# Kernel tuning notes

Measured on AMD Instinct MI355X. Metric: run time of the kernel, lower is better.

Reference implementation:

```python
import jax, jax.numpy as jnp
import numpy as np

N, E, P = 50000, 500000, 10000
F_IN, H, C = 128, 256, 1


def gat_conv(x, src, dst, W, a_s, a_d, b):
    # single-head GATConv (PyG): h = x W; e_ij = LeakyReLU(a_s.h_j + a_d.h_i)
    n = x.shape[0]
    h = x @ W                              # [n, out]
    es = h @ a_s                           # [n]
    ed = h @ a_d                           # [n]
    logits = jax.nn.leaky_relu(es[src] + ed[dst], 0.2)   # [E']
    m = jax.ops.segment_max(logits, dst, num_segments=n)
    p = jnp.exp(logits - m[dst])
    denom = jax.ops.segment_sum(p, dst, num_segments=n)
    alpha = p / denom[dst]                 # edge-softmax over incoming edges
    out = jax.ops.segment_sum(h[src] * alpha[:, None], dst, num_segments=n)
    return out + b


def setup_inputs():
    key = jax.random.key(0)
    ks = jax.random.split(key, 14)
    inp = {
        "features": jax.random.normal(ks[0], (N, F_IN), jnp.float32),
        "edge_index": jax.random.randint(ks[1], (2, E), 0, N, dtype=jnp.int32),
        "mask": jax.random.randint(ks[2], (P, 2), 0, N, dtype=jnp.int32),
        "W1": jax.random.normal(ks[3], (F_IN, H), jnp.float32) / np.sqrt(F_IN),
        "a_src1": jax.random.normal(ks[4], (H,), jnp.float32) / np.sqrt(H),
        "a_dst1": jax.random.normal(ks[5], (H,), jnp.float32) / np.sqrt(H),
        "b1": jnp.zeros((H,), jnp.float32),
        "W2": jax.random.normal(ks[6], (H, F_IN), jnp.float32) / np.sqrt(H),
        "a_src2": jax.random.normal(ks[7], (F_IN,), jnp.float32) / np.sqrt(F_IN),
        "a_dst2": jax.random.normal(ks[8], (F_IN,), jnp.float32) / np.sqrt(F_IN),
        "b2": jnp.zeros((F_IN,), jnp.float32),
        "Wl": jax.random.normal(ks[9], (2 * F_IN, C), jnp.float32) / np.sqrt(2 * F_IN),
        "bl": jnp.zeros((C,), jnp.float32),
    }
    return inp


def reference(features, edge_index, mask, W1, a_src1, a_dst1, b1, W2, a_src2, a_dst2, b2, Wl, bl):
    n = features.shape[0]
    loop = jnp.arange(n, dtype=edge_index.dtype)   # PyG add_self_loops=True
    src = jnp.concatenate([edge_index[0], loop])
    dst = jnp.concatenate([edge_index[1], loop])
    h = gat_conv(features, src, dst, W1, a_src1, a_dst1, b1)   # [N, H]
    h = jax.nn.relu(h)                                         # dropout=0.0
    h = gat_conv(h, src, dst, W2, a_src2, a_dst2, b2)          # [N, F_IN]
    mT = mask.T
    p1 = jax.lax.stop_gradient(h[mT[0]])   # .detach() in original
    p2 = jax.lax.stop_gradient(h[mT[1]])
    z = jnp.concatenate([p1, p2], axis=1)  # [P, 2*F_IN]
    return jax.nn.sigmoid(z @ Wl + bl)
```

## Files before the change

### kernel.cpp

```cpp
#include <hip/hip_runtime.h>
#include <hip/hip_bf16.h>
#include <math.h>

#define NN 50000
#define NE 500000
#define NP 10000
#define FIN 128
#define HD 256
#define NE_TOT (NE + NN)

typedef __attribute__((ext_vector_type(8))) short bf16x8;
typedef __attribute__((ext_vector_type(4))) float f32x4;
typedef __attribute__((ext_vector_type(2))) float f32x2;

__device__ inline unsigned short f2bf(float f) {
  unsigned int u = __float_as_uint(f);
  unsigned int r = (u + 0x7fffu + ((u >> 16) & 1u)) >> 16;
  return (unsigned short)r;
}

__device__ inline float bflo(unsigned int u) { return __uint_as_float(u << 16); }
__device__ inline float bfhi(unsigned int u) { return __uint_as_float(u & 0xffff0000u); }

__device__ inline unsigned char f2fp8(float v) {
  int pk = __builtin_amdgcn_cvt_pk_fp8_f32(v, v, 0, false);
  return (unsigned char)(pk & 0xff);
}

__global__ void init_prep(int* __restrict__ deg,
                          const float* __restrict__ W1, const float* __restrict__ W2,
                          unsigned short* __restrict__ W1T, unsigned short* __restrict__ W2T) {
  int idx = blockIdx.x * 256 + threadIdx.x;
  if (idx < NN) deg[idx] = 1;
  if (idx < FIN * HD) {
    int n = idx / FIN, k = idx - n * FIN;
    W1T[idx] = f2bf(W1[(size_t)k * HD + n]);
    int n2 = idx / HD, k2 = idx - n2 * HD;
    W2T[idx] = f2bf(W2[(size_t)k2 * FIN + n2]);
  }
}

__global__ void hist_kernel(const int* __restrict__ dst, int* __restrict__ deg) {
  int e = blockIdx.x * blockDim.x + threadIdx.x;
  if (e < NE) atomicAdd(&deg[dst[e]], 1);
}

__global__ void scan_phase1(const int* __restrict__ deg, int* __restrict__ incl,
                            int* __restrict__ bsum, int n) {
  __shared__ int tmp[256];
  int i = blockIdx.x * 256 + threadIdx.x;
  int v = (i < n) ? deg[i] : 0;
  tmp[threadIdx.x] = v;
  __syncthreads();
  for (int off = 1; off < 256; off <<= 1) {
    int t = (threadIdx.x >= off) ? tmp[threadIdx.x - off] : 0;
    __syncthreads();
    tmp[threadIdx.x] += t;
    __syncthreads();
  }
  if (i < n) incl[i] = tmp[threadIdx.x];
  if (threadIdx.x == 255) bsum[blockIdx.x] = tmp[255];
}

__global__ void scan_phase3(const int* __restrict__ deg, const int* __restrict__ incl,
                            const int* __restrict__ bsum, int* __restrict__ row_ptr,
                            int* __restrict__ cursor, int n, int total, int nb) {
  __shared__ int wsum[4];
  int bid = blockIdx.x;
  int v = (threadIdx.x < bid && threadIdx.x < nb) ? bsum[threadIdx.x] : 0;
#pragma unroll
  for (int off = 32; off; off >>= 1) v += __shfl_xor(v, off, 64);
  if ((threadIdx.x & 63) == 0) wsum[threadIdx.x >> 6] = v;
  __syncthreads();
  int prefix = wsum[0] + wsum[1] + wsum[2] + wsum[3];

  int i = bid * 256 + threadIdx.x;
  if (i < n) {
    int excl = incl[i] - deg[i] + prefix;
    row_ptr[i] = excl;
    cursor[i] = excl;
  }
  if (i == n) row_ptr[n] = total;
}

__global__ void scatter_kernel(const int* __restrict__ src, const int* __restrict__ dst,
                               int* __restrict__ cursor, int* __restrict__ ssrc) {
  int e = blockIdx.x * blockDim.x + threadIdx.x;
  if (e < NE) {
    int pos = atomicAdd(&cursor[dst[e]], 1);
    ssrc[pos] = src[e];
  } else if (e < NE_TOT) {
    int i = e - NE;
    int pos = atomicAdd(&cursor[i], 1);
    ssrc[pos] = i;
  }
}

template <int BN, int KTOT, bool A_BF16, bool C_FP8>
__global__ __launch_bounds__(512)
void mfma_gemm(const void* __restrict__ Aptr, const unsigned short* __restrict__ BT,
               void* __restrict__ Cptr, const float* __restrict__ a_s,
               const float* __restrict__ a_d, float* __restrict__ es, float* __restrict__ ed,
               int M) {
  constexpr int LDK = 72;
  constexpr int CN = BN / 2;
  constexpr int NT = CN / 16;
  __shared__ unsigned short As[128][LDK];
  __shared__ unsigned short Bs[BN][LDK];
  __shared__ float esl[128][2];
  __shared__ float edl[128][2];
  const int tid = threadIdx.x;
  const int wave = tid >> 6;
  const int lane = tid & 63;
  const int quad = lane >> 4;
  const int l16 = lane & 15;
  const int wrow = wave >> 1;
  const int wcol = wave & 1;
  const int row0 = blockIdx.x * 128;

  f32x4 acc[2][NT] = {};

  for (int k0 = 0; k0 < KTOT; k0 += 64) {
#pragma unroll
    for (int p = 0; p < 4; p++) {
      int m = p * 32 + (tid >> 4);
      int k4 = (tid & 15) * 4;
      int gr = row0 + m;
      uint2 pk = make_uint2(0u, 0u);
      if (gr < M) {
        if (A_BF16) {
          pk = *(const uint2*)((const unsigned short*)Aptr + (size_t)gr * KTOT + k0 + k4);
        } else {
          float4 v = *(const float4*)((const float*)Aptr + (size_t)gr * KTOT + k0 + k4);
          pk.x = (unsigned int)f2bf(v.x) | ((unsigned int)f2bf(v.y) << 16);
          pk.y = (unsigned int)f2bf(v.z) | ((unsigned int)f2bf(v.w) << 16);
        }
      }
      *(uint2*)&As[m][k4] = pk;
    }
#pragma unroll
    for (int p = 0; p < BN / 64; p++) {
      int n = p * 64 + (tid >> 3);
      int k8 = (tid & 7) * 8;
      *(uint4*)&Bs[n][k8] = *(const uint4*)(BT + (size_t)n * KTOT + k0 + k8);
    }
    __syncthreads();
#pragma unroll
    for (int ks = 0; ks < 2; ks++) {
      bf16x8 afrag[2];
#pragma unroll
      for (int rt = 0; rt < 2; rt++)
        afrag[rt] = *(const bf16x8*)&As[wrow * 32 + rt * 16 + l16][ks * 32 + quad * 8];
#pragma unroll
      for (int ct = 0; ct < NT; ct++) {
        bf16x8 bfrag = *(const bf16x8*)&Bs[wcol * CN + ct * 16 + l16][ks * 32 + quad * 8];
#pragma unroll
        for (int rt = 0; rt < 2; rt++)
          acc[rt][ct] = __builtin_amdgcn_mfma_f32_16x16x32_bf16(afrag[rt], bfrag, acc[rt][ct], 0, 0, 0);
      }
    }
    __syncthreads();
  }

  float asv[NT], adv[NT];
#pragma unroll
  for (int ct = 0; ct < NT; ct++) {
    asv[ct] = a_s[wcol * CN + ct * 16 + l16];
    adv[ct] = a_d[wcol * CN + ct * 16 + l16];
  }
#pragma unroll
  for (int rt = 0; rt < 2; rt++) {
#pragma unroll
    for (int r = 0; r < 4; r++) {
      int lrow = wrow * 32 + rt * 16 + quad * 4 + r;
      int grow = row0 + lrow;
      bool ok = (grow < M);
      float ps = 0.f, pd = 0.f;
#pragma unroll
      for (int ct = 0; ct < NT; ct++) {
        float v = acc[rt][ct][r];
        ps += v * asv[ct];
        pd += v * adv[ct];
        if (ok) {
          size_t cidx = (size_t)grow * BN + wcol * CN + ct * 16 + l16;
          if (C_FP8) ((unsigned char*)Cptr)[cidx] = f2fp8(v);
          else       ((unsigned short*)Cptr)[cidx] = f2bf(v);
        }
      }
#pragma unroll
      for (int off = 1; off < 16; off <<= 1) {
        ps += __shfl_xor(ps, off, 16);
        pd += __shfl_xor(pd, off, 16);
      }
      if (l16 == 0) {
        esl[lrow][wcol] = ps;
        edl[lrow][wcol] = pd;
      }
    }
  }
  __syncthreads();
  if (tid < 128) {
    int grow = row0 + tid;
    if (grow < M) {
      es[grow] = esl[tid][0] + esl[tid][1];
      ed[grow] = edl[tid][0] + edl[tid][1];
    }
  }
}

__global__ __launch_bounds__(256)
void fused_agg64(const int* __restrict__ row_ptr, const int* __restrict__ ssrc,
                 const float* __restrict__ es, const float* __restrict__ ed,
                 const unsigned char* __restrict__ h, const float* __restrict__ bias,
                 unsigned short* __restrict__ outp, int n) {
  int i = blockIdx.x * 8 + (threadIdx.x >> 5);
  int ls = threadIdx.x & 31;
  if (i >= n) return;
  int s = row_ptr[i], e = row_ptr[i + 1];
  float edv = ed[i];

  int msrc0 = 0;
  float logit0 = -1e30f;
  {
    int p = s + ls;
    if (p < e) {
      msrc0 = ssrc[p];
      float t = es[msrc0] + edv;
      logit0 = (t > 0.f) ? t : 0.2f * t;
    }
  }
  float mloc = logit0;
  for (int p0 = s + 32; p0 < e; p0 += 32) {
    int p = p0 + ls;
    if (p < e) {
      int ms = ssrc[p];
      float t = es[ms] + edv;
      float lg = (t > 0.f) ? t : 0.2f * t;
      mloc = fmaxf(mloc, lg);
    }
  }
#pragma unroll
  for (int off = 16; off; off >>= 1) mloc = fmaxf(mloc, __shfl_xor(mloc, off, 32));

  float acc[8] = {};
  float lsum = 0.f;
  const unsigned char* hb = h + ls * 8;
  for (int p0 = s; p0 < e; p0 += 32) {
    int msrc;
    float logit;
    if (p0 == s) {
      msrc = msrc0;
      logit = logit0;
    } else {
      int p = p0 + ls;
      msrc = 0;
      logit = -1e30f;
      if (p < e) {
        msrc = ssrc[p];
        float t = es[msrc] + edv;
        logit = (t > 0.f) ? t : 0.2f * t;
      }
    }
    float pv = __expf(logit - mloc);
    lsum += pv;
    int cnt = min(32, e - p0);
    for (int j = 0; j < cnt; j += 8) {
      uint2 r[8];
      float w[8];
#pragma unroll
      for (int u = 0; u < 8; u++) {
        int jj = j + u;
        bool ok = jj < cnt;
        int jc = ok ? jj : 0;
        int sj = __shfl(msrc, jc, 32);
        float wr = __shfl(pv, jc, 32);
        w[u] = ok ? wr : 0.f;
        r[u] = *(const uint2*)(hb + (size_t)sj * HD);
      }
#pragma unroll
      for (int u = 0; u < 8; u++) {
        f32x2 lo, hi;
        lo = __builtin_amdgcn_cvt_pk_f32_fp8(r[u].x, false);
        hi = __builtin_amdgcn_cvt_pk_f32_fp8(r[u].x, true);
        acc[0] += w[u] * lo.x; acc[1] += w[u] * lo.y; acc[2] += w[u] * hi.x; acc[3] += w[u] * hi.y;
        lo = __builtin_amdgcn_cvt_pk_f32_fp8(r[u].y, false);
        hi = __builtin_amdgcn_cvt_pk_f32_fp8(r[u].y, true);
        acc[4] += w[u] * lo.x; acc[5] += w[u] * lo.y; acc[6] += w[u] * hi.x; acc[7] += w[u] * hi.y;
      }
    }
  }
#pragma unroll
  for (int off = 16; off; off >>= 1) lsum += __shfl_xor(lsum, off, 32);
  float invd = 1.0f / lsum;
  float4 b0 = *(const float4*)(bias + ls * 8 + 0);
  float4 b1 = *(const float4*)(bias + ls * 8 + 4);
  unsigned int pk0 = (unsigned int)f2bf(fmaxf(acc[0] * invd + b0.x, 0.f)) |
                     ((unsigned int)f2bf(fmaxf(acc[1] * invd + b0.y, 0.f)) << 16);
  unsigned int pk1 = (unsigned int)f2bf(fmaxf(acc[2] * invd + b0.z, 0.f)) |
                     ((unsigned int)f2bf(fmaxf(acc[3] * invd + b0.w, 0.f)) << 16);
  unsigned int pk2 = (unsigned int)f2bf(fmaxf(acc[4] * invd + b1.x, 0.f)) |
                     ((unsigned int)f2bf(fmaxf(acc[5] * invd + b1.y, 0.f)) << 16);
  unsigned int pk3 = (unsigned int)f2bf(fmaxf(acc[6] * invd + b1.w == b1.w ? acc[6] * invd + b1.z : 0.f, 0.f)) |
                     ((unsigned int)f2bf(fmaxf(acc[7] * invd + b1.w, 0.f)) << 16);
  pk3 = (unsigned int)f2bf(fmaxf(acc[6] * invd + b1.z, 0.f)) |
        ((unsigned int)f2bf(fmaxf(acc[7] * invd + b1.w, 0.f)) << 16);
  *(uint4*)(outp + (size_t)i * HD + ls * 8) = make_uint4(pk0, pk1, pk2, pk3);
}

__global__ __launch_bounds__(256)
void fused_agg_l2_pair(const int* __restrict__ row_ptr, const int* __restrict__ ssrc,
                       const float* __restrict__ es, const float* __restrict__ ed,
                       const unsigned short* __restrict__ h, const float* __restrict__ bias,
                       const int* __restrict__ mask, const float* __restrict__ Wl,
                       const float* __restrict__ bl, float* __restrict__ out, int P) {
  constexpr int F = FIN;
  int pair = blockIdx.x * 4 + (threadIdx.x >> 6);
  if (pair >= P) return;
  int lane = threadIdx.x & 63;
  int hf = lane >> 5;
  int ls = lane & 31;
  int i = mask[pair * 2 + hf];
  int s = row_ptr[i], e = row_ptr[i + 1];
  float edv = ed[i];

  int msrc0 = 0;
  float logit0 = -1e30f;
  {
    int p = s + ls;
    if (p < e) {
      msrc0 = ssrc[p];
      float t = es[msrc0] + edv;
      logit0 = (t > 0.f) ? t : 0.2f * t;
    }
  }
  float M = logit0;
  for (int p0 = s + 32; p0 < e; p0 += 32) {
    int p = p0 + ls;
    if (p < e) {
      int ms = ssrc[p];
      float t = es[ms] + edv;
      float lg = (t > 0.f) ? t : 0.2f * t;
      M = fmaxf(M, lg);
    }
  }
#pragma unroll
  for (int off = 16; off; off >>= 1) M = fmaxf(M, __shfl_xor(M, off, 32));

  float acc0 = 0.f, acc1 = 0.f, acc2 = 0.f, acc3 = 0.f;
  float lsum = 0.f;
  const unsigned short* hb = h + ls * 4;
  for (int p0 = s; p0 < e; p0 += 32) {
    int msrc;
    float logit;
    if (p0 == s) {
      msrc = msrc0;
      logit = logit0;
    } else {
      int p = p0 + ls;
      msrc = 0;
      logit = -1e30f;
      if (p < e) {
        msrc = ssrc[p];
        float t = es[msrc] + edv;
        logit = (t > 0.f) ? t : 0.2f * t;
      }
    }
    float pv = __expf(logit - M);
    lsum += pv;
    int cnt = min(32, e - p0);
    for (int j = 0; j < cnt; j += 8) {
      uint2 r[8];
      float w[8];
#pragma unroll
      for (int u = 0; u < 8; u++) {
        int jj = j + u;
        bool ok = jj < cnt;
        int jc = ok ? jj : 0;
        int sj = __shfl(msrc, jc, 32);
        float wr = __shfl(pv, jc, 32);
        w[u] = ok ? wr : 0.f;
        r[u] = *(const uint2*)(hb + (size_t)sj * F);
      }
#pragma unroll
      for (int u = 0; u < 8; u++) {
        acc0 += w[u] * bflo(r[u].x);
        acc1 += w[u] * bfhi(r[u].x);
        acc2 += w[u] * bflo(r[u].y);
        acc3 += w[u] * bfhi(r[u].y);
      }
    }
  }
#pragma unroll
  for (int off = 16; off; off >>= 1) lsum += __shfl_xor(lsum, off, 32);
  float invd = 1.0f / lsum;
  float4 b4 = *(const float4*)(bias + ls * 4);
  float4 w4 = *(const float4*)(Wl + hf * F + ls * 4);
  float dotv = (acc0 * invd + b4.x) * w4.x + (acc1 * invd + b4.y) * w4.y +
               (acc2 * invd + b4.z) * w4.z + (acc3 * invd + b4.w) * w4.w;
#pragma unroll
  for (int off = 16; off; off >>= 1) dotv += __shfl_xor(dotv, off, 32);
  float othr = __shfl(dotv, lane ^ 32, 64);
  if (lane == 0) {
    float z = dotv + othr + bl[0];
    out[pair] = 1.0f / (1.0f + expf(-z));
  }
}

extern "C" void kernel_launch(void* const* d_in, const int* in_sizes, int n_in,
                              void* d_out, int out_size, void* d_ws, size_t ws_size,
                              hipStream_t stream) {
  const float* features = (const float*)d_in[0];
  const int* edge_index = (const int*)d_in[1];
  const int* mask       = (const int*)d_in[2];
  const float* W1     = (const float*)d_in[3];
  const float* a_src1 = (const float*)d_in[4];
  const float* a_dst1 = (const float*)d_in[5];
  const float* b1     = (const float*)d_in[6];
  const float* W2     = (const float*)d_in[7];
  const float* a_src2 = (const float*)d_in[8];
  const float* a_dst2 = (const float*)d_in[9];
  const float* b2     = (const float*)d_in[10];
  const float* Wl     = (const float*)d_in[11];
  const float* bl     = (const float*)d_in[12];
  float* out = (float*)d_out;

  const int* src = edge_index;
  const int* dst = edge_index + NE;

  char* ws = (char*)d_ws;
  size_t off = 0;
  auto alloc = [&](size_t bytes) {
    void* p = ws + off;
    off += (bytes + 255) & ~(size_t)255;
    return p;
  };
  unsigned char* h1q = (unsigned char*)alloc((size_t)NN * HD);
  unsigned short* h2b = (unsigned short*)alloc((size_t)NN * FIN * 2);
  unsigned short* x2b = (unsigned short*)alloc((size_t)NN * HD * 2);
  unsigned short* W1T = (unsigned short*)alloc((size_t)HD * FIN * 2);
  unsigned short* W2T = (unsigned short*)alloc((size_t)FIN * HD * 2);
  float* es_buf  = (float*)alloc((size_t)NN * 4);
  float* ed_buf  = (float*)alloc((size_t)NN * 4);
  int* deg       = (int*)alloc((size_t)NN * 4);
  int* incl      = (int*)alloc((size_t)NN * 4);
  int* bsum      = (int*)alloc(1024);
  int* row_ptr   = (int*)alloc((size_t)(NN + 1) * 4);
  int* cursor    = (int*)alloc((size_t)NN * 4);
  int* ssrc      = (int*)alloc((size_t)NE_TOT * 4);
  (void)ws_size; (void)in_sizes; (void)n_in; (void)out_size;

  const int nblk_gemm = (NN + 127) / 128;
  const int nblk_n256 = (NN + 255) / 256;

  init_prep<<<nblk_n256, 256, 0, stream>>>(deg, W1, W2, W1T, W2T);
  hist_kernel<<<(NE + 255) / 256, 256, 0, stream>>>(dst, deg);
  scan_phase1<<<nblk_n256, 256, 0, stream>>>(deg, incl, bsum, NN);
  scan_phase3<<<nblk_n256 + 1, 256, 0, stream>>>(
      deg, incl, bsum, row_ptr, cursor, NN, NE_TOT, nblk_n256);
  scatter_kernel<<<(NE_TOT + 255) / 256, 256, 0, stream>>>(src, dst, cursor, ssrc);

  mfma_gemm<HD, FIN, false, true><<<nblk_gemm, 512, 0, stream>>>(
      (const void*)features, W1T, (void*)h1q, a_src1, a_dst1, es_buf, ed_buf, NN);
  fused_agg64<<<(NN + 7) / 8, 256, 0, stream>>>(
      row_ptr, ssrc, es_buf, ed_buf, h1q, b1, x2b, NN);

  mfma_gemm<FIN, HD, true, false><<<nblk_gemm, 512, 0, stream>>>(
      (const void*)x2b, W2T, (void*)h2b, a_src2, a_dst2, es_buf, ed_buf, NN);
  fused_agg_l2_pair<<<(NP + 3) / 4, 256, 0, stream>>>(
      row_ptr, ssrc, es_buf, ed_buf, h2b, b2, mask, Wl, bl, out, NP);
}
```

Before: 221.3 us.

## Fuse CSR scatter into first GEMM launch and drop softmax max pass

```diff
diff --git a/kernel.cpp b/kernel.cpp
--- a/kernel.cpp
+++ b/kernel.cpp
@@ -8,6 +8,7 @@
 #define FIN 128
 #define HD 256
 #define NE_TOT (NE + NN)
+#define NBG 391
 
 typedef __attribute__((ext_vector_type(8))) short bf16x8;
 typedef __attribute__((ext_vector_type(4))) float f32x4;
@@ -83,16 +84,129 @@
   if (i == n) row_ptr[n] = total;
 }
 
-__global__ void scatter_kernel(const int* __restrict__ src, const int* __restrict__ dst,
-                               int* __restrict__ cursor, int* __restrict__ ssrc) {
-  int e = blockIdx.x * blockDim.x + threadIdx.x;
-  if (e < NE) {
-    int pos = atomicAdd(&cursor[dst[e]], 1);
-    ssrc[pos] = src[e];
-  } else if (e < NE_TOT) {
-    int i = e - NE;
-    int pos = atomicAdd(&cursor[i], 1);
-    ssrc[pos] = i;
+template <int BN, int KTOT, bool A_BF16, bool C_FP8>
+__global__ __launch_bounds__(512)
+void gemm_scatter(const void* __restrict__ Aptr, const unsigned short* __restrict__ BT,
+                  void* __restrict__ Cptr, const float* __restrict__ a_s,
+                  const float* __restrict__ a_d, float* __restrict__ es, float* __restrict__ ed,
+                  int M, const int* __restrict__ src, const int* __restrict__ dst,
+                  const int* __restrict__ row_ptr, int* __restrict__ cursor,
+                  int* __restrict__ ssrc) {
+  if (blockIdx.x >= NBG) {
+    int e = (blockIdx.x - NBG) * 512 + threadIdx.x;
+    if (e < NE) {
+      int d = dst[e];
+      int pos = atomicAdd(&cursor[d], 1);
+      ssrc[pos] = src[e];
+    } else if (e < NE_TOT) {
+      int i = e - NE;
+      ssrc[row_ptr[i + 1] - 1] = i;
+    }
+    return;
+  }
+  constexpr int LDK = 72;
+  constexpr int CN = BN / 2;
+  constexpr int NT = CN / 16;
+  __shared__ unsigned short As[128][LDK];
+  __shared__ unsigned short Bs[BN][LDK];
+  __shared__ float esl[128][2];
+  __shared__ float edl[128][2];
+  const int tid = threadIdx.x;
+  const int wave = tid >> 6;
+  const int lane = tid & 63;
+  const int quad = lane >> 4;
+  const int l16 = lane & 15;
+  const int wrow = wave >> 1;
+  const int wcol = wave & 1;
+  const int row0 = blockIdx.x * 128;
+
+  f32x4 acc[2][NT] = {};
+
+  for (int k0 = 0; k0 < KTOT; k0 += 64) {
+#pragma unroll
+    for (int p = 0; p < 4; p++) {
+      int m = p * 32 + (tid >> 4);
+      int k4 = (tid & 15) * 4;
+      int gr = row0 + m;
+      uint2 pk = make_uint2(0u, 0u);
+      if (gr < M) {
+        if (A_BF16) {
+          pk = *(const uint2*)((const unsigned short*)Aptr + (size_t)gr * KTOT + k0 + k4);
+        } else {
+          float4 v = *(const float4*)((const float*)Aptr + (size_t)gr * KTOT + k0 + k4);
+          pk.x = (unsigned int)f2bf(v.x) | ((unsigned int)f2bf(v.y) << 16);
+          pk.y = (unsigned int)f2bf(v.z) | ((unsigned int)f2bf(v.w) << 16);
+        }
+      }
+      *(uint2*)&As[m][k4] = pk;
+    }
+#pragma unroll
+    for (int p = 0; p < BN / 64; p++) {
+      int n = p * 64 + (tid >> 3);
+      int k8 = (tid & 7) * 8;
+      *(uint4*)&Bs[n][k8] = *(const uint4*)(BT + (size_t)n * KTOT + k0 + k8);
+    }
+    __syncthreads();
+#pragma unroll
+    for (int ks = 0; ks < 2; ks++) {
+      bf16x8 afrag[2];
+#pragma unroll
+      for (int rt = 0; rt < 2; rt++)
+        afrag[rt] = *(const bf16x8*)&As[wrow * 32 + rt * 16 + l16][ks * 32 + quad * 8];
+#pragma unroll
+      for (int ct = 0; ct < NT; ct++) {
+        bf16x8 bfrag = *(const bf16x8*)&Bs[wcol * CN + ct * 16 + l16][ks * 32 + quad * 8];
+#pragma unroll
+        for (int rt = 0; rt < 2; rt++)
+          acc[rt][ct] = __builtin_amdgcn_mfma_f32_16x16x32_bf16(afrag[rt], bfrag, acc[rt][ct], 0, 0, 0);
+      }
+    }
+    __syncthreads();
+  }
+
+  float asv[NT], adv[NT];
+#pragma unroll
+  for (int ct = 0; ct < NT; ct++) {
+    asv[ct] = a_s[wcol * CN + ct * 16 + l16];
+    adv[ct] = a_d[wcol * CN + ct * 16 + l16];
+  }
+#pragma unroll
+  for (int rt = 0; rt < 2; rt++) {
+#pragma unroll
+    for (int r = 0; r < 4; r++) {
+      int lrow = wrow * 32 + rt * 16 + quad * 4 + r;
+      int grow = row0 + lrow;
+      bool ok = (grow < M);
+      float ps = 0.f, pd = 0.f;
+#pragma unroll
+      for (int ct = 0; ct < NT; ct++) {
+        float v = acc[rt][ct][r];
+        ps += v * asv[ct];
+        pd += v * adv[ct];
+        if (ok) {
+          size_t cidx = (size_t)grow * BN + wcol * CN + ct * 16 + l16;
+          if (C_FP8) ((unsigned char*)Cptr)[cidx] = f2fp8(v);
+          else       ((unsigned short*)Cptr)[cidx] = f2bf(v);
+        }
+      }
+#pragma unroll
+      for (int off = 1; off < 16; off <<= 1) {
+        ps += __shfl_xor(ps, off, 16);
+        pd += __shfl_xor(pd, off, 16);
+      }
+      if (l16 == 0) {
+        esl[lrow][wcol] = ps;
+        edl[lrow][wcol] = pd;
+      }
+    }
+  }
+  __syncthreads();
+  if (tid < 128) {
+    int grow = row0 + tid;
+    if (grow < M) {
+      es[grow] = esl[tid][0] + esl[tid][1];
+      ed[grow] = edl[tid][0] + edl[tid][1];
+    }
   }
 }
 
@@ -219,49 +333,19 @@
   int s = row_ptr[i], e = row_ptr[i + 1];
   float edv = ed[i];
 
-  int msrc0 = 0;
-  float logit0 = -1e30f;
-  {
-    int p = s + ls;
-    if (p < e) {
-      msrc0 = ssrc[p];
-      float t = es[msrc0] + edv;
-      logit0 = (t > 0.f) ? t : 0.2f * t;
-    }
-  }
-  float mloc = logit0;
-  for (int p0 = s + 32; p0 < e; p0 += 32) {
-    int p = p0 + ls;
-    if (p < e) {
-      int ms = ssrc[p];
-      float t = es[ms] + edv;
-      float lg = (t > 0.f) ? t : 0.2f * t;
-      mloc = fmaxf(mloc, lg);
-    }
-  }
-#pragma unroll
-  for (int off = 16; off; off >>= 1) mloc = fmaxf(mloc, __shfl_xor(mloc, off, 32));
-
   float acc[8] = {};
   float lsum = 0.f;
   const unsigned char* hb = h + ls * 8;
   for (int p0 = s; p0 < e; p0 += 32) {
-    int msrc;
-    float logit;
-    if (p0 == s) {
-      msrc = msrc0;
-      logit = logit0;
-    } else {
-      int p = p0 + ls;
-      msrc = 0;
-      logit = -1e30f;
-      if (p < e) {
-        msrc = ssrc[p];
-        float t = es[msrc] + edv;
-        logit = (t > 0.f) ? t : 0.2f * t;
-      }
-    }
-    float pv = __expf(logit - mloc);
+    int p = p0 + ls;
+    int msrc = 0;
+    float pv = 0.f;
+    if (p < e) {
+      msrc = ssrc[p];
+      float t = es[msrc] + edv;
+      float lg = (t > 0.f) ? t : 0.2f * t;
+      pv = __expf(lg);
+    }
     lsum += pv;
     int cnt = min(32, e - p0);
     for (int j = 0; j < cnt; j += 8) {
@@ -300,10 +384,8 @@
                      ((unsigned int)f2bf(fmaxf(acc[3] * invd + b0.w, 0.f)) << 16);
   unsigned int pk2 = (unsigned int)f2bf(fmaxf(acc[4] * invd + b1.x, 0.f)) |
                      ((unsigned int)f2bf(fmaxf(acc[5] * invd + b1.y, 0.f)) << 16);
-  unsigned int pk3 = (unsigned int)f2bf(fmaxf(acc[6] * invd + b1.w == b1.w ? acc[6] * invd + b1.z : 0.f, 0.f)) |
+  unsigned int pk3 = (unsigned int)f2bf(fmaxf(acc[6] * invd + b1.z, 0.f)) |
                      ((unsigned int)f2bf(fmaxf(acc[7] * invd + b1.w, 0.f)) << 16);
-  pk3 = (unsigned int)f2bf(fmaxf(acc[6] * invd + b1.z, 0.f)) |
-        ((unsigned int)f2bf(fmaxf(acc[7] * invd + b1.w, 0.f)) << 16);
   *(uint4*)(outp + (size_t)i * HD + ls * 8) = make_uint4(pk0, pk1, pk2, pk3);
 }
 
@@ -323,49 +405,19 @@
   int s = row_ptr[i], e = row_ptr[i + 1];
   float edv = ed[i];
 
-  int msrc0 = 0;
-  float logit0 = -1e30f;
-  {
-    int p = s + ls;
-    if (p < e) {
-      msrc0 = ssrc[p];
-      float t = es[msrc0] + edv;
-      logit0 = (t > 0.f) ? t : 0.2f * t;
-    }
-  }
-  float M = logit0;
-  for (int p0 = s + 32; p0 < e; p0 += 32) {
-    int p = p0 + ls;
-    if (p < e) {
-      int ms = ssrc[p];
-      float t = es[ms] + edv;
-      float lg = (t > 0.f) ? t : 0.2f * t;
-      M = fmaxf(M, lg);
-    }
-  }
-#pragma unroll
-  for (int off = 16; off; off >>= 1) M = fmaxf(M, __shfl_xor(M, off, 32));
-
   float acc0 = 0.f, acc1 = 0.f, acc2 = 0.f, acc3 = 0.f;
   float lsum = 0.f;
   const unsigned short* hb = h + ls * 4;
   for (int p0 = s; p0 < e; p0 += 32) {
-    int msrc;
-    float logit;
-    if (p0 == s) {
-      msrc = msrc0;
-      logit = logit0;
-    } else {
-      int p = p0 + ls;
-      msrc = 0;
-      logit = -1e30f;
-      if (p < e) {
-        msrc = ssrc[p];
-        float t = es[msrc] + edv;
-        logit = (t > 0.f) ? t : 0.2f * t;
-      }
-    }
-    float pv = __expf(logit - M);
+    int p = p0 + ls;
+    int msrc = 0;
+    float pv = 0.f;
+    if (p < e) {
+      msrc = ssrc[p];
+      float t = es[msrc] + edv;
+      float lg = (t > 0.f) ? t : 0.2f * t;
+      pv = __expf(lg);
+    }
     lsum += pv;
     int cnt = min(32, e - p0);
     for (int j = 0; j < cnt; j += 8) {
@@ -449,22 +501,20 @@
   int* ssrc      = (int*)alloc((size_t)NE_TOT * 4);
   (void)ws_size; (void)in_sizes; (void)n_in; (void)out_size;
 
-  const int nblk_gemm = (NN + 127) / 128;
   const int nblk_n256 = (NN + 255) / 256;
+  const int nblk_scat = (NE_TOT + 511) / 512;
 
   init_prep<<<nblk_n256, 256, 0, stream>>>(deg, W1, W2, W1T, W2T);
   hist_kernel<<<(NE + 255) / 256, 256, 0, stream>>>(dst, deg);
   scan_phase1<<<nblk_n256, 256, 0, stream>>>(deg, incl, bsum, NN);
   scan_phase3<<<nblk_n256 + 1, 256, 0, stream>>>(
       deg, incl, bsum, row_ptr, cursor, NN, NE_TOT, nblk_n256);
-  scatter_kernel<<<(NE_TOT + 255) / 256, 256, 0, stream>>>(src, dst, cursor, ssrc);
-
-  mfma_gemm<HD, FIN, false, true><<<nblk_gemm, 512, 0, stream>>>(
-      (const void*)features, W1T, (void*)h1q, a_src1, a_dst1, es_buf, ed_buf, NN);
+  gemm_scatter<HD, FIN, false, true><<<NBG + nblk_scat, 512, 0, stream>>>(
+      (const void*)features, W1T, (void*)h1q, a_src1, a_dst1, es_buf, ed_buf, NN,
+      src, dst, row_ptr, cursor, ssrc);
   fused_agg64<<<(NN + 7) / 8, 256, 0, stream>>>(
       row_ptr, ssrc, es_buf, ed_buf, h1q, b1, x2b, NN);
-
-  mfma_gemm<FIN, HD, true, false><<<nblk_gemm, 512, 0, stream>>>(
+  mfma_gemm<FIN, HD, true, false><<<(NN + 127) / 128, 512, 0, stream>>>(
       (const void*)x2b, W2T, (void*)h2b, a_src2, a_dst2, es_buf, ed_buf, NN);
   fused_agg_l2_pair<<<(NP + 3) / 4, 256, 0, stream>>>(
       row_ptr, ssrc, es_buf, ed_buf, h2b, b2, mask, Wl, bl, out, NP);
```

Result: faster. 215.3 us (-2.7%).
